# Kernel optimization log

Measured on AMD Instinct MI355X. Metric: run time of the kernel, lower is better.

Reference implementation:

```python
import jax, jax.numpy as jnp
import numpy as np

NUM_HEADS = 4
WINDOW = 64  # 8*8


def setup_inputs() -> dict:
    key = jax.random.key(0)
    ks = jax.random.split(key, 8)
    C = 128
    x = jax.random.normal(ks[0], (16, C, 128, 128), dtype=jnp.float32)
    s = 0.02
    Wq = jax.random.normal(ks[1], (C, C), dtype=jnp.float32) * s
    bq = jax.random.normal(ks[2], (C,), dtype=jnp.float32) * s
    Wk = jax.random.normal(ks[3], (C, C), dtype=jnp.float32) * s
    bk = jax.random.normal(ks[4], (C,), dtype=jnp.float32) * s
    Wv = jax.random.normal(ks[5], (C, C), dtype=jnp.float32) * s
    bv = jax.random.normal(ks[6], (C,), dtype=jnp.float32) * s
    Bbias = jnp.zeros((WINDOW, WINDOW), dtype=jnp.float32)
    return {"x": x, "Wq": Wq, "bq": bq, "Wk": Wk, "bk": bk, "Wv": Wv, "bv": bv, "Bbias": Bbias}


def reference(x, Wq, bq, Wk, bk, Wv, bv, Bbias):
    B, C, H, W = x.shape
    nW = (H * W) // WINDOW
    h = NUM_HEADS
    d = C // h
    # (B,C,H,W) -> (B,H,W,C) -> (B, nW, WINDOW, C)
    xr = jnp.transpose(x, (0, 2, 3, 1)).reshape(B, nW, WINDOW, C)
    # torch Linear: y = x @ W.T + b
    q = xr @ Wq.T + bq
    k = xr @ Wk.T + bk
    v = xr @ Wv.T + bv
    # split heads: (B, nW, WINDOW, h, d) -> (B, nW, h, WINDOW, d)
    def split(t):
        return jnp.transpose(t.reshape(B, nW, WINDOW, h, d), (0, 1, 3, 2, 4))
    Q, K, V = split(q), split(k), split(v)
    scale = 1.0 / jnp.sqrt(jnp.asarray(d, dtype=x.dtype))
    scores = jnp.einsum('bnhqd,bnhkd->bnhqk', Q, K) * scale + Bbias
    probs = jax.nn.softmax(scores, axis=-1)
    out = jnp.einsum('bnhqk,bnhkd->bnhqd', probs, V)
    # (B, nW, h, WINDOW, d) -> (B, nW, WINDOW, C) -> (B,H,W,C) -> (B,C,H,W)
    out = jnp.transpose(out, (0, 1, 3, 2, 4)).reshape(B, H, W, C)
    return jnp.transpose(out, (0, 3, 1, 2))
```

## Files before the change

### kernel.cpp

```cpp
#include <hip/hip_runtime.h>
#include <hip/hip_bf16.h>


typedef __attribute__((ext_vector_type(8))) short bf16x8;
typedef __attribute__((ext_vector_type(4))) short bf16x4;
typedef __attribute__((ext_vector_type(4))) float f32x4;

#define MFMA32(A, B, C) __builtin_amdgcn_mfma_f32_16x16x32_bf16((A), (B), (C), 0, 0, 0)
#define MFMA16(A, B, C) __builtin_amdgcn_mfma_f32_16x16x16bf16_1k((A), (B), (C), 0, 0, 0)

__device__ __forceinline__ ushort f2bf(float f) {
    __hip_bfloat16 h = __float2bfloat16(f);
    ushort u; __builtin_memcpy(&u, &h, 2); return u;
}
__device__ __forceinline__ unsigned pk2(float a, float b) {
    __hip_bfloat162 h = __float22bfloat162_rn(make_float2(a, b));
    unsigned u; __builtin_memcpy(&u, &h, 4); return u;
}
__device__ __forceinline__ bf16x4 pk4(float a, float b, float c, float d) {
    uint2 u; u.x = pk2(a, b); u.y = pk2(c, d);
    bf16x4 r; __builtin_memcpy(&r, &u, 8); return r;
}
__device__ __forceinline__ int fsw(int row) { return ((row ^ (row >> 4)) & 15) << 4; }

__global__ void wconv(const float* __restrict__ Wq, const float* __restrict__ Wk,
                      const float* __restrict__ Wv, ushort* __restrict__ out) {
    int i = blockIdx.x * 256 + threadIdx.x;
    out[i]         = f2bf(Wq[i]);
    out[16384 + i] = f2bf(Wk[i]);
    out[32768 + i] = f2bf(Wv[i]);
}

__global__ __launch_bounds__(256, 2)
void attn_win(const float* __restrict__ x, const ushort* __restrict__ wbf,
              const float* __restrict__ bq, const float* __restrict__ bk,
              const float* __restrict__ bv, const float* __restrict__ Bb,
              float* __restrict__ out) {
    __shared__ __align__(16) char sX[16384];

    const int tid = threadIdx.x;
    const int w = tid >> 6;
    const int l = tid & 63;
    const int lr = l & 15;
    const int lg = (l >> 4) & 3;
    const int blk = blockIdx.x;
    const int b = blk >> 8, n = blk & 255;
    const long xbase = (long)b * 128 * 16384 + n * 64;

    #pragma unroll
    for (int it = 0; it < 2; ++it) {
        int idx = it * 256 + tid;
        int cq = idx >> 4, t4 = idx & 15;
        const float* px = x + xbase + (long)(4 * cq) * 16384 + t4 * 4;
        float4 v0 = *(const float4*)(px);
        float4 v1 = *(const float4*)(px + 16384);
        float4 v2 = *(const float4*)(px + 32768);
        float4 v3 = *(const float4*)(px + 49152);
        float a0[4] = {v0.x, v0.y, v0.z, v0.w};
        float a1[4] = {v1.x, v1.y, v1.z, v1.w};
        float a2[4] = {v2.x, v2.y, v2.z, v2.w};
        float a3[4] = {v3.x, v3.y, v3.z, v3.w};
        #pragma unroll
        for (int jj = 0; jj < 4; ++jj) {
            int t = t4 * 4 + jj;
            uint2 pk;
            pk.x = pk2(a0[jj], a1[jj]);
            pk.y = pk2(a2[jj], a3[jj]);
            *(uint2*)(sX + t * 256 + ((8 * cq) ^ fsw(t))) = pk;
        }
    }
    __syncthreads();

    bf16x4 fQ[4][2], fK[4][2];
    bf16x4 fV[4][2];
    {
        f32x4 accQ[2][4], accK[2][4], accV[4][2];
        #pragma unroll
        for (int tn = 0; tn < 2; ++tn) {
            float4 bbq = *(const float4*)(bq + 32 * w + 16 * tn + 4 * lg);
            float4 bbk = *(const float4*)(bk + 32 * w + 16 * tn + 4 * lg);
            float bvv = bv[32 * w + 16 * tn + lr];
            #pragma unroll
            for (int tm = 0; tm < 4; ++tm) {
                accQ[tn][tm] = (f32x4){bbq.x, bbq.y, bbq.z, bbq.w};
                accK[tn][tm] = (f32x4){bbk.x, bbk.y, bbk.z, bbk.w};
                accV[tm][tn] = (f32x4){bvv, bvv, bvv, bvv};
            }
        }
        #pragma unroll
        for (int kk = 0; kk < 4; ++kk) {
            bf16x8 aXk[4];
            #pragma unroll
            for (int tm = 0; tm < 4; ++tm) {
                int row = 16 * tm + lr;
                aXk[tm] = *(const bf16x8*)(sX + row * 256
                              + (((8 * lg + 32 * kk) * 2) ^ fsw(row)));
            }
            bf16x8 bWq[2], bWk[2], bWv[2];
            #pragma unroll
            for (int tn = 0; tn < 2; ++tn) {
                int orow = (32 * w + 16 * tn + lr) * 128 + 8 * lg + 32 * kk;
                bWq[tn] = *(const bf16x8*)(wbf + orow);
                bWk[tn] = *(const bf16x8*)(wbf + 16384 + orow);
                bWv[tn] = *(const bf16x8*)(wbf + 32768 + orow);
            }
            #pragma unroll
            for (int tn = 0; tn < 2; ++tn)
                #pragma unroll
                for (int tm = 0; tm < 4; ++tm) {
                    accQ[tn][tm] = MFMA32(bWq[tn], aXk[tm], accQ[tn][tm]);
                    accK[tn][tm] = MFMA32(bWk[tn], aXk[tm], accK[tn][tm]);
                    accV[tm][tn] = MFMA32(aXk[tm], bWv[tn], accV[tm][tn]);
                }
        }
        #pragma unroll
        for (int tm = 0; tm < 4; ++tm)
            #pragma unroll
            for (int tn = 0; tn < 2; ++tn) {
                fQ[tm][tn] = pk4(accQ[tn][tm][0], accQ[tn][tm][1],
                                 accQ[tn][tm][2], accQ[tn][tm][3]);
                fK[tm][tn] = pk4(accK[tn][tm][0], accK[tn][tm][1],
                                 accK[tn][tm][2], accK[tn][tm][3]);
                fV[tm][tn] = pk4(accV[tm][tn][0], accV[tm][tn][1],
                                 accV[tm][tn][2], accV[tm][tn][3]);
            }
    }

    const float scale = 0.17677669529663687f;
    const float L2E = 1.4426950408889634f;
    bf16x4 pP[4][4];
    #pragma unroll
    for (int tmQ = 0; tmQ < 4; ++tmQ) {
        f32x4 sc[4];
        #pragma unroll
        for (int tmK = 0; tmK < 4; ++tmK) {
            sc[tmK] = (f32x4){0.f, 0.f, 0.f, 0.f};
            sc[tmK] = MFMA16(fK[tmK][0], fQ[tmQ][0], sc[tmK]);
            sc[tmK] = MFMA16(fK[tmK][1], fQ[tmQ][1], sc[tmK]);
        }
        int q = 16 * tmQ + lr;
        float s = 0.f;
        #pragma unroll
        for (int tmK = 0; tmK < 4; ++tmK) {
            float4 bb = *(const float4*)(Bb + q * 64 + 16 * tmK + 4 * lg);
            float e0 = exp2f((sc[tmK][0] * scale + bb.x) * L2E);
            float e1 = exp2f((sc[tmK][1] * scale + bb.y) * L2E);
            float e2 = exp2f((sc[tmK][2] * scale + bb.z) * L2E);
            float e3 = exp2f((sc[tmK][3] * scale + bb.w) * L2E);
            sc[tmK][0] = e0; sc[tmK][1] = e1;
            sc[tmK][2] = e2; sc[tmK][3] = e3;
            s += (e0 + e1) + (e2 + e3);
        }
        s += __shfl_xor(s, 16);
        s += __shfl_xor(s, 32);
        float rs = 1.0f / s;
        #pragma unroll
        for (int tmK = 0; tmK < 4; ++tmK)
            pP[tmK][tmQ] = pk4(sc[tmK][0] * rs, sc[tmK][1] * rs,
                               sc[tmK][2] * rs, sc[tmK][3] * rs);
    }

    f32x4 o[4][2];
    #pragma unroll
    for (int tmq = 0; tmq < 4; ++tmq)
        #pragma unroll
        for (int tn = 0; tn < 2; ++tn)
            o[tmq][tn] = (f32x4){0.f, 0.f, 0.f, 0.f};
    #pragma unroll
    for (int tmK = 0; tmK < 4; ++tmK)
        #pragma unroll
        for (int tmq = 0; tmq < 4; ++tmq)
            #pragma unroll
            for (int tn = 0; tn < 2; ++tn)
                o[tmq][tn] = MFMA16(pP[tmK][tmq], fV[tmK][tn], o[tmq][tn]);

    #pragma unroll
    for (int tmq = 0; tmq < 4; ++tmq)
        #pragma unroll
        for (int tn = 0; tn < 2; ++tn) {
            int ch = 32 * w + 16 * tn + lr;
            int tok = 16 * tmq + 4 * lg;
            float4 ov;
            ov.x = o[tmq][tn][0];
            ov.y = o[tmq][tn][1];
            ov.z = o[tmq][tn][2];
            ov.w = o[tmq][tn][3];
            *(float4*)(out + xbase + (long)ch * 16384 + tok) = ov;
        }
}

extern "C" void kernel_launch(void* const* d_in, const int* in_sizes, int n_in,
                              void* d_out, int out_size, void* d_ws, size_t ws_size,
                              hipStream_t stream) {
    const float* x  = (const float*)d_in[0];
    const float* Wq = (const float*)d_in[1];
    const float* bq = (const float*)d_in[2];
    const float* Wk = (const float*)d_in[3];
    const float* bk = (const float*)d_in[4];
    const float* Wv = (const float*)d_in[5];
    const float* bv = (const float*)d_in[6];
    const float* Bb = (const float*)d_in[7];
    float* out = (float*)d_out;
    ushort* wbf = (ushort*)d_ws;

    wconv<<<64, 256, 0, stream>>>(Wq, Wk, Wv, wbf);
    attn_win<<<4096, 256, 0, stream>>>(x, wbf, bq, bk, bv, Bb, out);
}
```

Baseline: 111.5 us.

## Process eight windows per block with double-buffered register prefetch of next window

```diff
diff --git a/kernel.cpp b/kernel.cpp
--- a/kernel.cpp
+++ b/kernel.cpp
@@ -36,22 +36,24 @@
               const float* __restrict__ bq, const float* __restrict__ bk,
               const float* __restrict__ bv, const float* __restrict__ Bb,
               float* __restrict__ out) {
-    __shared__ __align__(16) char sX[16384];
+    __shared__ __align__(16) char sX[2][16384];
 
     const int tid = threadIdx.x;
     const int w = tid >> 6;
     const int l = tid & 63;
     const int lr = l & 15;
     const int lg = (l >> 4) & 3;
-    const int blk = blockIdx.x;
-    const int b = blk >> 8, n = blk & 255;
-    const long xbase = (long)b * 128 * 16384 + n * 64;
+    const int g = blockIdx.x;
+    const int win0 = g * 8;
+    const long xbB = (long)(win0 >> 8) * 128 * 16384 + (long)(win0 & 255) * 64;
+
+    const int cq_s = tid >> 4, t4_s = tid & 15;
 
     #pragma unroll
     for (int it = 0; it < 2; ++it) {
         int idx = it * 256 + tid;
         int cq = idx >> 4, t4 = idx & 15;
-        const float* px = x + xbase + (long)(4 * cq) * 16384 + t4 * 4;
+        const float* px = x + xbB + (long)(4 * cq) * 16384 + t4 * 4;
         float4 v0 = *(const float4*)(px);
         float4 v1 = *(const float4*)(px + 16384);
         float4 v2 = *(const float4*)(px + 32768);
@@ -66,127 +68,169 @@
             uint2 pk;
             pk.x = pk2(a0[jj], a1[jj]);
             pk.y = pk2(a2[jj], a3[jj]);
-            *(uint2*)(sX + t * 256 + ((8 * cq) ^ fsw(t))) = pk;
+            *(uint2*)(&sX[0][0] + t * 256 + ((8 * cq) ^ fsw(t))) = pk;
         }
     }
     __syncthreads();
 
-    bf16x4 fQ[4][2], fK[4][2];
-    bf16x4 fV[4][2];
-    {
-        f32x4 accQ[2][4], accK[2][4], accV[4][2];
-        #pragma unroll
-        for (int tn = 0; tn < 2; ++tn) {
-            float4 bbq = *(const float4*)(bq + 32 * w + 16 * tn + 4 * lg);
-            float4 bbk = *(const float4*)(bk + 32 * w + 16 * tn + 4 * lg);
-            float bvv = bv[32 * w + 16 * tn + lr];
-            #pragma unroll
-            for (int tm = 0; tm < 4; ++tm) {
-                accQ[tn][tm] = (f32x4){bbq.x, bbq.y, bbq.z, bbq.w};
-                accK[tn][tm] = (f32x4){bbk.x, bbk.y, bbk.z, bbk.w};
-                accV[tm][tn] = (f32x4){bvv, bvv, bvv, bvv};
-            }
-        }
-        #pragma unroll
-        for (int kk = 0; kk < 4; ++kk) {
-            bf16x8 aXk[4];
-            #pragma unroll
-            for (int tm = 0; tm < 4; ++tm) {
-                int row = 16 * tm + lr;
-                aXk[tm] = *(const bf16x8*)(sX + row * 256
-                              + (((8 * lg + 32 * kk) * 2) ^ fsw(row)));
-            }
-            bf16x8 bWq[2], bWk[2], bWv[2];
+    #pragma unroll 1
+    for (int wi = 0; wi < 8; ++wi) {
+        const int cur = wi & 1, nxt = cur ^ 1;
+        const char* sXw = &sX[cur][0];
+        const long xb = xbB + wi * 64;
+
+        float4 pf[2][4];
+        if (wi < 7) {
+            #pragma unroll
+            for (int it = 0; it < 2; ++it) {
+                int idx = it * 256 + tid;
+                int cq = idx >> 4, t4 = idx & 15;
+                const float* px = x + xb + 64 + (long)(4 * cq) * 16384 + t4 * 4;
+                pf[it][0] = *(const float4*)(px);
+                pf[it][1] = *(const float4*)(px + 16384);
+                pf[it][2] = *(const float4*)(px + 32768);
+                pf[it][3] = *(const float4*)(px + 49152);
+            }
+        }
+
+        bf16x4 fQ[4][2], fK[4][2], fV[4][2];
+        {
+            f32x4 accQ[2][4], accK[2][4], accV[4][2];
             #pragma unroll
             for (int tn = 0; tn < 2; ++tn) {
-                int orow = (32 * w + 16 * tn + lr) * 128 + 8 * lg + 32 * kk;
-                bWq[tn] = *(const bf16x8*)(wbf + orow);
-                bWk[tn] = *(const bf16x8*)(wbf + 16384 + orow);
-                bWv[tn] = *(const bf16x8*)(wbf + 32768 + orow);
-            }
+                float4 bbq = *(const float4*)(bq + 32 * w + 16 * tn + 4 * lg);
+                float4 bbk = *(const float4*)(bk + 32 * w + 16 * tn + 4 * lg);
+                float bvv = bv[32 * w + 16 * tn + lr];
+                #pragma unroll
+                for (int tm = 0; tm < 4; ++tm) {
+                    accQ[tn][tm] = (f32x4){bbq.x, bbq.y, bbq.z, bbq.w};
+                    accK[tn][tm] = (f32x4){bbk.x, bbk.y, bbk.z, bbk.w};
+                    accV[tm][tn] = (f32x4){bvv, bvv, bvv, bvv};
+                }
+            }
+            #pragma unroll
+            for (int kk = 0; kk < 4; ++kk) {
+                bf16x8 aXk[4];
+                #pragma unroll
+                for (int tm = 0; tm < 4; ++tm) {
+                    int row = 16 * tm + lr;
+                    aXk[tm] = *(const bf16x8*)(sXw + row * 256
+                                  + (((8 * lg + 32 * kk) * 2) ^ fsw(row)));
+                }
+                bf16x8 bWq[2], bWk[2], bWv[2];
+                #pragma unroll
+                for (int tn = 0; tn < 2; ++tn) {
+                    int orow = (32 * w + 16 * tn + lr) * 128 + 8 * lg + 32 * kk;
+                    bWq[tn] = *(const bf16x8*)(wbf + orow);
+                    bWk[tn] = *(const bf16x8*)(wbf + 16384 + orow);
+                    bWv[tn] = *(const bf16x8*)(wbf + 32768 + orow);
+                }
+                #pragma unroll
+                for (int tn = 0; tn < 2; ++tn)
+                    #pragma unroll
+                    for (int tm = 0; tm < 4; ++tm) {
+                        accQ[tn][tm] = MFMA32(bWq[tn], aXk[tm], accQ[tn][tm]);
+                        accK[tn][tm] = MFMA32(bWk[tn], aXk[tm], accK[tn][tm]);
+                        accV[tm][tn] = MFMA32(aXk[tm], bWv[tn], accV[tm][tn]);
+                    }
+            }
+            #pragma unroll
+            for (int tm = 0; tm < 4; ++tm)
+                #pragma unroll
+                for (int tn = 0; tn < 2; ++tn) {
+                    fQ[tm][tn] = pk4(accQ[tn][tm][0], accQ[tn][tm][1],
+                                     accQ[tn][tm][2], accQ[tn][tm][3]);
+                    fK[tm][tn] = pk4(accK[tn][tm][0], accK[tn][tm][1],
+                                     accK[tn][tm][2], accK[tn][tm][3]);
+                    fV[tm][tn] = pk4(accV[tm][tn][0], accV[tm][tn][1],
+                                     accV[tm][tn][2], accV[tm][tn][3]);
+                }
+        }
+
+        const float scale = 0.17677669529663687f;
+        const float L2E = 1.4426950408889634f;
+        bf16x4 pP[4][4];
+        #pragma unroll
+        for (int tmQ = 0; tmQ < 4; ++tmQ) {
+            f32x4 sc[4];
+            #pragma unroll
+            for (int tmK = 0; tmK < 4; ++tmK) {
+                sc[tmK] = (f32x4){0.f, 0.f, 0.f, 0.f};
+                sc[tmK] = MFMA16(fK[tmK][0], fQ[tmQ][0], sc[tmK]);
+                sc[tmK] = MFMA16(fK[tmK][1], fQ[tmQ][1], sc[tmK]);
+            }
+            int q = 16 * tmQ + lr;
+            float s = 0.f;
+            #pragma unroll
+            for (int tmK = 0; tmK < 4; ++tmK) {
+                float4 bb = *(const float4*)(Bb + q * 64 + 16 * tmK + 4 * lg);
+                float e0 = exp2f((sc[tmK][0] * scale + bb.x) * L2E);
+                float e1 = exp2f((sc[tmK][1] * scale + bb.y) * L2E);
+                float e2 = exp2f((sc[tmK][2] * scale + bb.z) * L2E);
+                float e3 = exp2f((sc[tmK][3] * scale + bb.w) * L2E);
+                sc[tmK][0] = e0; sc[tmK][1] = e1;
+                sc[tmK][2] = e2; sc[tmK][3] = e3;
+                s += (e0 + e1) + (e2 + e3);
+            }
+            s += __shfl_xor(s, 16);
+            s += __shfl_xor(s, 32);
+            float rs = 1.0f / s;
+            #pragma unroll
+            for (int tmK = 0; tmK < 4; ++tmK)
+                pP[tmK][tmQ] = pk4(sc[tmK][0] * rs, sc[tmK][1] * rs,
+                                   sc[tmK][2] * rs, sc[tmK][3] * rs);
+        }
+
+        f32x4 o[4][2];
+        #pragma unroll
+        for (int tmq = 0; tmq < 4; ++tmq)
             #pragma unroll
             for (int tn = 0; tn < 2; ++tn)
-                #pragma unroll
-                for (int tm = 0; tm < 4; ++tm) {
-                    accQ[tn][tm] = MFMA32(bWq[tn], aXk[tm], accQ[tn][tm]);
-                    accK[tn][tm] = MFMA32(bWk[tn], aXk[tm], accK[tn][tm]);
-                    accV[tm][tn] = MFMA32(aXk[tm], bWv[tn], accV[tm][tn]);
-                }
-        }
-        #pragma unroll
-        for (int tm = 0; tm < 4; ++tm)
+                o[tmq][tn] = (f32x4){0.f, 0.f, 0.f, 0.f};
+        #pragma unroll
+        for (int tmK = 0; tmK < 4; ++tmK)
+            #pragma unroll
+            for (int tmq = 0; tmq < 4; ++tmq)
+                #pragma unroll
+                for (int tn = 0; tn < 2; ++tn)
+                    o[tmq][tn] = MFMA16(pP[tmK][tmq], fV[tmK][tn], o[tmq][tn]);
+
+        #pragma unroll
+        for (int tmq = 0; tmq < 4; ++tmq)
             #pragma unroll
             for (int tn = 0; tn < 2; ++tn) {
-                fQ[tm][tn] = pk4(accQ[tn][tm][0], accQ[tn][tm][1],
-                                 accQ[tn][tm][2], accQ[tn][tm][3]);
-                fK[tm][tn] = pk4(accK[tn][tm][0], accK[tn][tm][1],
-                                 accK[tn][tm][2], accK[tn][tm][3]);
-                fV[tm][tn] = pk4(accV[tm][tn][0], accV[tm][tn][1],
-                                 accV[tm][tn][2], accV[tm][tn][3]);
-            }
+                int ch = 32 * w + 16 * tn + lr;
+                int tok = 16 * tmq + 4 * lg;
+                float4 ov;
+                ov.x = o[tmq][tn][0];
+                ov.y = o[tmq][tn][1];
+                ov.z = o[tmq][tn][2];
+                ov.w = o[tmq][tn][3];
+                *(float4*)(out + xb + (long)ch * 16384 + tok) = ov;
+            }
+
+        if (wi < 7) {
+            #pragma unroll
+            for (int it = 0; it < 2; ++it) {
+                int idx = it * 256 + tid;
+                int cq = idx >> 4, t4 = idx & 15;
+                float a0[4] = {pf[it][0].x, pf[it][0].y, pf[it][0].z, pf[it][0].w};
+                float a1[4] = {pf[it][1].x, pf[it][1].y, pf[it][1].z, pf[it][1].w};
+                float a2[4] = {pf[it][2].x, pf[it][2].y, pf[it][2].z, pf[it][2].w};
+                float a3[4] = {pf[it][3].x, pf[it][3].y, pf[it][3].z, pf[it][3].w};
+                #pragma unroll
+                for (int jj = 0; jj < 4; ++jj) {
+                    int t = t4 * 4 + jj;
+                    uint2 pk;
+                    pk.x = pk2(a0[jj], a1[jj]);
+                    pk.y = pk2(a2[jj], a3[jj]);
+                    *(uint2*)(&sX[nxt][0] + t * 256 + ((8 * cq) ^ fsw(t))) = pk;
+                }
+            }
+        }
+        __syncthreads();
     }
-
-    const float scale = 0.17677669529663687f;
-    const float L2E = 1.4426950408889634f;
-    bf16x4 pP[4][4];
-    #pragma unroll
-    for (int tmQ = 0; tmQ < 4; ++tmQ) {
-        f32x4 sc[4];
-        #pragma unroll
-        for (int tmK = 0; tmK < 4; ++tmK) {
-            sc[tmK] = (f32x4){0.f, 0.f, 0.f, 0.f};
-            sc[tmK] = MFMA16(fK[tmK][0], fQ[tmQ][0], sc[tmK]);
-            sc[tmK] = MFMA16(fK[tmK][1], fQ[tmQ][1], sc[tmK]);
-        }
-        int q = 16 * tmQ + lr;
-        float s = 0.f;
-        #pragma unroll
-        for (int tmK = 0; tmK < 4; ++tmK) {
-            float4 bb = *(const float4*)(Bb + q * 64 + 16 * tmK + 4 * lg);
-            float e0 = exp2f((sc[tmK][0] * scale + bb.x) * L2E);
-            float e1 = exp2f((sc[tmK][1] * scale + bb.y) * L2E);
-            float e2 = exp2f((sc[tmK][2] * scale + bb.z) * L2E);
-            float e3 = exp2f((sc[tmK][3] * scale + bb.w) * L2E);
-            sc[tmK][0] = e0; sc[tmK][1] = e1;
-            sc[tmK][2] = e2; sc[tmK][3] = e3;
-            s += (e0 + e1) + (e2 + e3);
-        }
-        s += __shfl_xor(s, 16);
-        s += __shfl_xor(s, 32);
-        float rs = 1.0f / s;
-        #pragma unroll
-        for (int tmK = 0; tmK < 4; ++tmK)
-            pP[tmK][tmQ] = pk4(sc[tmK][0] * rs, sc[tmK][1] * rs,
-                               sc[tmK][2] * rs, sc[tmK][3] * rs);
-    }
-
-    f32x4 o[4][2];
-    #pragma unroll
-    for (int tmq = 0; tmq < 4; ++tmq)
-        #pragma unroll
-        for (int tn = 0; tn < 2; ++tn)
-            o[tmq][tn] = (f32x4){0.f, 0.f, 0.f, 0.f};
-    #pragma unroll
-    for (int tmK = 0; tmK < 4; ++tmK)
-        #pragma unroll
-        for (int tmq = 0; tmq < 4; ++tmq)
-            #pragma unroll
-            for (int tn = 0; tn < 2; ++tn)
-                o[tmq][tn] = MFMA16(pP[tmK][tmq], fV[tmK][tn], o[tmq][tn]);
-
-    #pragma unroll
-    for (int tmq = 0; tmq < 4; ++tmq)
-        #pragma unroll
-        for (int tn = 0; tn < 2; ++tn) {
-            int ch = 32 * w + 16 * tn + lr;
-            int tok = 16 * tmq + 4 * lg;
-            float4 ov;
-            ov.x = o[tmq][tn][0];
-            ov.y = o[tmq][tn][1];
-            ov.z = o[tmq][tn][2];
-            ov.w = o[tmq][tn][3];
-            *(float4*)(out + xbase + (long)ch * 16384 + tok) = ov;
-        }
+    (void)cq_s; (void)t4_s;
 }
 
 extern "C" void kernel_launch(void* const* d_in, const int* in_sizes, int n_in,
@@ -204,5 +248,5 @@
     ushort* wbf = (ushort*)d_ws;
 
     wconv<<<64, 256, 0, stream>>>(Wq, Wk, Wv, wbf);
-    attn_win<<<4096, 256, 0, stream>>>(x, wbf, bq, bk, bv, Bb, out);
-}
+    attn_win<<<512, 256, 0, stream>>>(x, wbf, bq, bk, bv, Bb, out);
+}
```

After: 248.1 us. 122% more time.
